# Kernel tuning notes

Hardware: AMD Instinct MI355X
Metric: run time of the kernel (lower is better)

The kernel has to match this reference:

```python
import jax, jax.numpy as jnp
import numpy as np

# ---- static config (from grid_conf / data_aug_conf) ----
B, N, C = 4, 6, 64            # batch, cameras, camC
OGH, OGW = 256, 704           # final_dim
DOWN = 16                     # 32 // up_scale
FH, FW = OGH // DOWN, OGW // DOWN   # 16, 44
DB0, DB1, DBS = 4.0, 45.0, 1.0      # dbound
D = int((DB1 - DB0) / DBS)          # 41 depth bins
DX = np.array([0.5, 0.5, 20.0], np.float32)            # dx
BX = np.array([-49.75, -49.75, 0.0], np.float32)        # bx (lower + dx/2)
NX = (200, 200, 1)                                       # nx


def make_frustum():
    # [D, FH, FW, 3] pixel (u, v, depth) frustum, matches torch create_frustum
    ds = jnp.arange(DB0, DB1, DBS, dtype=jnp.float32)[:, None, None] * jnp.ones((1, FH, FW), jnp.float32)
    xs = jnp.linspace(0.0, OGW - 1.0, FW, dtype=jnp.float32)[None, None, :] * jnp.ones((D, FH, 1), jnp.float32)
    ys = jnp.linspace(0.0, OGH - 1.0, FH, dtype=jnp.float32)[None, :, None] * jnp.ones((D, 1, FW), jnp.float32)
    return jnp.stack([xs, ys, ds], axis=-1)


def get_geometry(rots, trans, intrins, post_rots, post_trans):
    # frustum points -> ego frame, [B, N, D, FH, FW, 3]
    pts = make_frustum()[None, None] - post_trans[:, :, None, None, None, :]
    pts = jnp.einsum('bnij,bndhwj->bndhwi', jnp.linalg.inv(post_rots), pts)
    # un-project: (u*d, v*d, d)
    pts = jnp.concatenate([pts[..., :2] * pts[..., 2:3], pts[..., 2:3]], axis=-1)
    combine = rots @ jnp.linalg.inv(intrins)
    return jnp.einsum('bnij,bndhwj->bndhwi', combine, pts) + trans[:, :, None, None, None, :]


def voxel_pooling(geom, x):
    # geom: [B,N,D,H,W,3] ego coords; x: [B,N,D,H,W,C] lifted features
    dx = jnp.asarray(DX); bx = jnp.asarray(BX)
    # voxel indices; .astype(int32) truncates toward zero like torch .long()
    gi = ((geom - (bx - dx / 2.0)) / dx).astype(jnp.int32)
    Np = B * N * D * FH * FW
    gi = gi.reshape(Np, 3)
    xf = x.reshape(Np, C)
    bidx = jnp.repeat(jnp.arange(B, dtype=jnp.int32), N * D * FH * FW)
    valid = ((gi[:, 0] >= 0) & (gi[:, 0] < NX[0]) &
             (gi[:, 1] >= 0) & (gi[:, 1] < NX[1]) &
             (gi[:, 2] >= 0) & (gi[:, 2] < NX[2]))
    # flat voxel id: (((b*nz + z)*nx0 + xi)*nx1 + yi)
    flat = ((bidx * NX[2] + gi[:, 2]) * NX[0] + gi[:, 0]) * NX[1] + gi[:, 1]
    flat = jnp.where(valid, flat, 0)
    xf = xf * valid[:, None].astype(xf.dtype)
    nvox = B * NX[2] * NX[0] * NX[1]
    # scatter-add == sort + cumsum-trick per-voxel sum in the torch code
    final = jax.ops.segment_sum(xf, flat, num_segments=nvox)          # [nvox, C]
    final = final.reshape(B, NX[2], NX[0], NX[1], C)
    final = jnp.transpose(final, (0, 1, 4, 2, 3)).reshape(B, NX[2] * C, NX[0], NX[1])
    return final


def setup_inputs() -> dict:
    key = jax.random.key(0)
    k1, k2 = jax.random.split(key)
    feat_depth = jax.random.normal(k1, (B, N, D, FH, FW), jnp.float32)
    feat_pv = jax.random.normal(k2, (B, N, C, FH, FW), jnp.float32)
    # realistic 6-camera nuScenes-like rig, intrinsics scaled to 704x256
    base = np.array([[0., 0., 1.], [-1., 0., 0.], [0., -1., 0.]], np.float32)  # cam axes -> ego axes
    rots = np.zeros((B, N, 3, 3), np.float32)
    trans = np.zeros((B, N, 3), np.float32)
    for n in range(N):
        yaw = 2.0 * np.pi * n / N
        Rz = np.array([[np.cos(yaw), -np.sin(yaw), 0.], [np.sin(yaw), np.cos(yaw), 0.], [0., 0., 1.]], np.float32)
        rots[:, n] = Rz @ base
        trans[:, n] = Rz @ np.array([1.5, 0.0, 1.6], np.float32)
    fx = 1266.0 * (OGW / 1600.0)
    intr = np.array([[fx, 0., OGW / 2.0], [0., fx, OGH / 2.0], [0., 0., 1.]], np.float32)
    return {
        'feat_depth': feat_depth,
        'feat_pv': feat_pv,
        'rots': jnp.asarray(rots),
        'trans': jnp.asarray(trans),
        'intrins': jnp.asarray(np.broadcast_to(intr, (B, N, 3, 3)).copy()),
        'post_rots': jnp.asarray(np.broadcast_to(np.eye(3, dtype=np.float32), (B, N, 3, 3)).copy()),
        'post_trans': jnp.zeros((B, N, 3), jnp.float32),
    }


def reference(feat_depth, feat_pv, rots, trans, intrins, post_rots, post_trans):
    geom = get_geometry(rots, trans, intrins, post_rots, post_trans)
    geom = jax.lax.stop_gradient(geom)  # torch casts to .long(): indices are non-diff
    depth = jax.nn.softmax(feat_depth, axis=2)                 # get_depth_dist over D
    # lift: depth.unsqueeze(1) * feat.unsqueeze(2) -> [B,N,D,C,H,W] -> [B,N,D,H,W,C]
    x = depth[:, :, :, None] * feat_pv[:, :, None]
    x = jnp.transpose(x, (0, 1, 2, 4, 5, 3))
    return voxel_pooling(geom, x)                               # [B, C*nz, 200, 200]
```

## Files before the change

### kernel.cpp

```cpp
#include <hip/hip_runtime.h>
#include <math.h>

namespace {
constexpr int kB = 4, kN = 6, kC = 64, kD = 41, kFH = 16, kFW = 44;
constexpr int kNX0 = 200, kNX1 = 200;
constexpr int kHW  = kFH * kFW;
constexpr int kPix = kB * kN * kHW;
constexpr int kPts = kPix * kD;
constexpr int kVox = kB * kNX0 * kNX1;
constexpr int kPvElems = kPix * kC;
constexpr int kScanBlks = kVox / 256;
constexpr int kPvtTiles = kPix / 64;
constexpr int kSmBlks = kPix / 256;
constexpr int kFrontBlks = kPvtTiles + kSmBlks + kScanBlks;

constexpr size_t kOffPvT    = 0;
constexpr size_t kSzPvT     = (size_t)kPvElems * 4;
constexpr size_t kOffWgt    = kOffPvT + kSzPvT;
constexpr size_t kSzWgt     = (size_t)kPts * 4;
constexpr size_t kOffCnt    = kOffWgt + kSzWgt;
constexpr size_t kSzCnt     = (size_t)kVox * 4;
constexpr size_t kOffOffs   = kOffCnt + kSzCnt;
constexpr size_t kSzOffs    = 640256;
constexpr size_t kOffBSum   = kOffOffs + kSzOffs;
constexpr size_t kSzBSum    = 2560;
constexpr size_t kOffBase   = kOffBSum + kSzBSum;
constexpr size_t kSzBase    = 2560;
constexpr size_t kOffTick   = kOffBase + kSzBase;
constexpr size_t kSzTick    = 256;
constexpr size_t kOffSKW    = kOffTick + kSzTick;
constexpr size_t kSzSKW     = (size_t)kPts * 8;
constexpr size_t kWsNeed    = kOffSKW + kSzSKW + 256;
}

__device__ __forceinline__ void inv3x3(const float m[9], float inv[9]) {
    float a = m[0], b = m[1], c = m[2];
    float d = m[3], e = m[4], f = m[5];
    float g = m[6], h = m[7], i = m[8];
    float A =  (e * i - f * h);
    float Bm = -(d * i - f * g);
    float Cm =  (d * h - e * g);
    float det = a * A + b * Bm + c * Cm;
    float r = 1.0f / det;
    inv[0] = A * r;
    inv[1] = -(b * i - c * h) * r;
    inv[2] =  (b * f - c * e) * r;
    inv[3] = Bm * r;
    inv[4] =  (a * i - c * g) * r;
    inv[5] = -(a * f - c * d) * r;
    inv[6] = Cm * r;
    inv[7] = -(a * h - b * g) * r;
    inv[8] =  (a * e - b * d) * r;
}

__device__ __forceinline__ int geo_flat(int q,
                                        const float* __restrict__ rots,
                                        const float* __restrict__ trans,
                                        const float* __restrict__ intrins,
                                        const float* __restrict__ post_rots,
                                        const float* __restrict__ post_trans) {
    const int bn  = q / (kD * kHW);
    const int rem = q - bn * (kD * kHW);
    const int d   = rem / kHW;
    const int hw  = rem - d * kHW;
    const int h   = hw / kFW;
    const int w   = hw - h * kFW;
    const int b   = bn / kN;

    const float* R  = rots       + bn * 9;
    const float* K  = intrins    + bn * 9;
    const float* PR = post_rots  + bn * 9;
    const float* PT = post_trans + bn * 3;
    const float* T  = trans      + bn * 3;

    float Km[9], PRm[9];
#pragma unroll
    for (int i = 0; i < 9; ++i) { Km[i] = K[i]; PRm[i] = PR[i]; }
    float invK[9], invPR[9];
    inv3x3(Km, invK);
    inv3x3(PRm, invPR);
    float M[9];
#pragma unroll
    for (int i = 0; i < 3; ++i)
#pragma unroll
        for (int j = 0; j < 3; ++j)
            M[i * 3 + j] = R[i * 3 + 0] * invK[0 * 3 + j]
                         + R[i * 3 + 1] * invK[1 * 3 + j]
                         + R[i * 3 + 2] * invK[2 * 3 + j];

    const float u  = (float)w * (703.0f / 43.0f);
    const float v  = (float)h * 17.0f;
    const float dv = 4.0f + (float)d;
    const float px = u - PT[0], py = v - PT[1], pz = dv - PT[2];
    const float ax = invPR[0] * px + invPR[1] * py + invPR[2] * pz;
    const float ay = invPR[3] * px + invPR[4] * py + invPR[5] * pz;
    const float az = invPR[6] * px + invPR[7] * py + invPR[8] * pz;
    const float qx = ax * az, qy = ay * az, qz = az;
    const float gx = M[0] * qx + M[1] * qy + M[2] * qz + T[0];
    const float gy = M[3] * qx + M[4] * qy + M[5] * qz + T[1];
    const float gz = M[6] * qx + M[7] * qy + M[8] * qz + T[2];
    const float fx = (gx + 50.0f) / 0.5f;
    const float fy = (gy + 50.0f) / 0.5f;
    const float fz = (gz + 10.0f) / 20.0f;
    const int gix = (int)fx;
    const int giy = (int)fy;
    const int giz = (int)fz;
    if (gix >= 0 && gix < kNX0 && giy >= 0 && giy < kNX1 && giz == 0)
        return (b * kNX0 + gix) * kNX1 + giy;
    return -1;
}

__global__ __launch_bounds__(256) void lss_front(const float* __restrict__ pv,
                                                 const float* __restrict__ feat_depth,
                                                 float* __restrict__ pvT,
                                                 float* __restrict__ wgtArr,
                                                 unsigned* __restrict__ counts,
                                                 unsigned* __restrict__ ticket) {
    __shared__ float t[64][65];
    const int blk = blockIdx.x;
    const int tid = threadIdx.x;
    if (blk == 0 && tid == 0) *ticket = 0u;

    if (blk < kPvtTiles) {
        const int pix0 = blk * 64;
        const int bn  = pix0 / kHW;
        const int hw0 = pix0 - bn * kHW;
        const int lane = tid & 63;
        const int wv   = tid >> 6;
        const float* src = pv + (size_t)(bn * kC) * kHW + hw0;
#pragma unroll
        for (int cc = 0; cc < 16; ++cc) {
            const int c = wv * 16 + cc;
            t[c][lane] = src[(size_t)c * kHW + lane];
        }
        __syncthreads();
        float* dst = pvT + (size_t)pix0 * kC;
#pragma unroll
        for (int jj = 0; jj < 16; ++jj) {
            const int j = wv * 16 + jj;
            dst[j * kC + lane] = t[lane][j];
        }
    } else if (blk < kPvtTiles + kSmBlks) {
        const int pix = (blk - kPvtTiles) * 256 + tid;
        const int bn = pix / kHW;
        const int hw = pix - bn * kHW;
        const float* p = feat_depth + (size_t)(bn * kD) * kHW + hw;
        float v[kD];
#pragma unroll
        for (int d = 0; d < kD; ++d) v[d] = p[(size_t)d * kHW];
        float mx = v[0];
#pragma unroll
        for (int d = 1; d < kD; ++d) mx = fmaxf(mx, v[d]);
        float sm = 0.0f;
#pragma unroll
        for (int d = 0; d < kD; ++d) { v[d] = __expf(v[d] - mx); sm += v[d]; }
        const float inv = 1.0f / sm;
        float* o = wgtArr + (size_t)(bn * kD) * kHW + hw;
#pragma unroll
        for (int d = 0; d < kD; ++d) o[(size_t)d * kHW] = v[d] * inv;
    } else {
        const int ci = (blk - kPvtTiles - kSmBlks) * 256 + tid;
        counts[ci] = 0u;
    }
}

__global__ __launch_bounds__(256) void lss_geo(
    const float* __restrict__ rots,
    const float* __restrict__ trans,
    const float* __restrict__ intrins,
    const float* __restrict__ post_rots,
    const float* __restrict__ post_trans,
    unsigned* __restrict__ counts)
{
    const int q = blockIdx.x * 256 + threadIdx.x;
    const int f = geo_flat(q, rots, trans, intrins, post_rots, post_trans);
    if (f >= 0) atomicAdd(&counts[f], 1u);
}

__global__ __launch_bounds__(256) void lss_scan(const unsigned* __restrict__ counts,
                                                unsigned* __restrict__ offsets,
                                                unsigned* __restrict__ blockSums,
                                                unsigned* __restrict__ bases,
                                                unsigned* __restrict__ ticket) {
    __shared__ unsigned wsum[4];
    __shared__ int lastFlag;
    const int tid = threadIdx.x;
    const int i = blockIdx.x * 256 + tid;
    const int lane = tid & 63;
    const int wv = tid >> 6;

    const unsigned c = counts[i];
    unsigned s = c;
#pragma unroll
    for (int o = 1; o < 64; o <<= 1) {
        unsigned v = __shfl_up(s, o);
        if (lane >= o) s += v;
    }
    if (lane == 63) wsum[wv] = s;
    __syncthreads();
    unsigned base = 0;
#pragma unroll
    for (int k = 0; k < 3; ++k)
        if (k < wv) base += wsum[k];
    const unsigned incl = s + base;
    offsets[i] = incl - c;
    if (tid == 255) {
        atomicExch(&blockSums[blockIdx.x], incl);
        __threadfence();
    }
    __syncthreads();
    if (tid == 0)
        lastFlag = (atomicAdd(ticket, 1u) == (unsigned)(kScanBlks - 1));
    __syncthreads();
    if (!lastFlag) return;

    __threadfence();
    const int lo = tid * 3;
    const unsigned c0 = (lo     < kScanBlks) ? blockSums[lo]     : 0u;
    const unsigned c1 = (lo + 1 < kScanBlks) ? blockSums[lo + 1] : 0u;
    const unsigned c2 = (lo + 2 < kScanBlks) ? blockSums[lo + 2] : 0u;
    const unsigned t3 = c0 + c1 + c2;
    unsigned si = t3;
#pragma unroll
    for (int o = 1; o < 64; o <<= 1) {
        unsigned v = __shfl_up(si, o);
        if (lane >= o) si += v;
    }
    __syncthreads();
    if (lane == 63) wsum[wv] = si;
    __syncthreads();
    unsigned b2 = 0;
#pragma unroll
    for (int k = 0; k < 3; ++k)
        if (k < wv) b2 += wsum[k];
    unsigned run = si - t3 + b2;
    if (lo     < kScanBlks) { bases[lo]     = run; run += c0; }
    if (lo + 1 < kScanBlks) { bases[lo + 1] = run; run += c1; }
    if (lo + 2 < kScanBlks) { bases[lo + 2] = run; run += c2; }
}

__global__ __launch_bounds__(256) void lss_order(
    const float* __restrict__ rots,
    const float* __restrict__ trans,
    const float* __restrict__ intrins,
    const float* __restrict__ post_rots,
    const float* __restrict__ post_trans,
    const float* __restrict__ wgtArr,
    unsigned* __restrict__ offsets,
    const unsigned* __restrict__ bases,
    uint2* __restrict__ skw)
{
    const int q = blockIdx.x * 256 + threadIdx.x;
    const int f = geo_flat(q, rots, trans, intrins, post_rots, post_trans);
    if (f >= 0) {
        const unsigned slot = atomicAdd(&offsets[f], 1u) + bases[f >> 8];
        const int bn  = q / (kD * kHW);
        const int rem = q - bn * (kD * kHW);
        const int hw  = rem % kHW;
        uint2 u;
        u.x = (unsigned)(bn * kHW + hw);
        u.y = __float_as_uint(wgtArr[q]);
        skw[slot] = u;
    }
}

__global__ __launch_bounds__(512) void lss_gather(const float* __restrict__ pvT,
                                                  const unsigned* __restrict__ offsets,
                                                  const unsigned* __restrict__ bases,
                                                  const uint2* __restrict__ skw,
                                                  float* __restrict__ out) {
    constexpr int kChunk = 2048;
    __shared__ float acc[50][65];
    __shared__ uint2 sbuf[kChunk];
    __shared__ unsigned rowOff[51];
    const int tile = blockIdx.x;
    const int yt = tile & 3;
    const int xi = (tile >> 2) % kNX0;
    const int b  = tile / (kNX0 * 4);
    const int yi0 = yt * 50;
    const int lane = threadIdx.x & 63;
    const int wave = threadIdx.x >> 6;
    const int flat0 = (b * kNX0 + xi) * kNX1 + yi0;

    for (int e = threadIdx.x; e < 50 * 65; e += 512)
        ((float*)acc)[e] = 0.0f;
    if (threadIdx.x < 51) {
        const int f = flat0 - 1 + (int)threadIdx.x;
        rowOff[threadIdx.x] = (f < 0) ? 0u : (offsets[f] + bases[f >> 8]);
    }
    __syncthreads();

    const unsigned seg0 = rowOff[0];
    const unsigned seg1 = rowOff[50];

    for (unsigned cb = seg0; cb < seg1; cb += (unsigned)kChunk) {
        const unsigned ce = min(cb + (unsigned)kChunk, seg1);
        const int n = (int)(ce - cb);
        for (int e = threadIdx.x; e < n; e += 512)
            sbuf[e] = skw[cb + e];
        __syncthreads();

        for (int j = wave; j < 50; j += 8) {
            unsigned s0 = max(rowOff[j], cb);
            unsigned e0 = min(rowOff[j + 1], ce);
            if (s0 >= e0) continue;
            float a0 = 0.0f, a1 = 0.0f, a2 = 0.0f, a3 = 0.0f;
            int p  = (int)(s0 - cb);
            int pe = (int)(e0 - cb);
            for (; p + 8 <= pe; p += 8) {
                const uint2 u0 = sbuf[p + 0];
                const uint2 u1 = sbuf[p + 1];
                const uint2 u2 = sbuf[p + 2];
                const uint2 u3 = sbuf[p + 3];
                const uint2 u4 = sbuf[p + 4];
                const uint2 u5 = sbuf[p + 5];
                const uint2 u6 = sbuf[p + 6];
                const uint2 u7 = sbuf[p + 7];
                const float* r0 = pvT + (size_t)((unsigned)__builtin_amdgcn_readfirstlane(u0.x)) * kC;
                const float* r1 = pvT + (size_t)((unsigned)__builtin_amdgcn_readfirstlane(u1.x)) * kC;
                const float* r2 = pvT + (size_t)((unsigned)__builtin_amdgcn_readfirstlane(u2.x)) * kC;
                const float* r3 = pvT + (size_t)((unsigned)__builtin_amdgcn_readfirstlane(u3.x)) * kC;
                const float* r4 = pvT + (size_t)((unsigned)__builtin_amdgcn_readfirstlane(u4.x)) * kC;
                const float* r5 = pvT + (size_t)((unsigned)__builtin_amdgcn_readfirstlane(u5.x)) * kC;
                const float* r6 = pvT + (size_t)((unsigned)__builtin_amdgcn_readfirstlane(u6.x)) * kC;
                const float* r7 = pvT + (size_t)((unsigned)__builtin_amdgcn_readfirstlane(u7.x)) * kC;
                const float f0 = r0[lane], f1 = r1[lane], f2 = r2[lane], f3 = r3[lane];
                const float f4 = r4[lane], f5 = r5[lane], f6 = r6[lane], f7 = r7[lane];
                a0 = fmaf(__uint_as_float(__builtin_amdgcn_readfirstlane(u0.y)), f0, a0);
                a1 = fmaf(__uint_as_float(__builtin_amdgcn_readfirstlane(u1.y)), f1, a1);
                a2 = fmaf(__uint_as_float(__builtin_amdgcn_readfirstlane(u2.y)), f2, a2);
                a3 = fmaf(__uint_as_float(__builtin_amdgcn_readfirstlane(u3.y)), f3, a3);
                a0 = fmaf(__uint_as_float(__builtin_amdgcn_readfirstlane(u4.y)), f4, a0);
                a1 = fmaf(__uint_as_float(__builtin_amdgcn_readfirstlane(u5.y)), f5, a1);
                a2 = fmaf(__uint_as_float(__builtin_amdgcn_readfirstlane(u6.y)), f6, a2);
                a3 = fmaf(__uint_as_float(__builtin_amdgcn_readfirstlane(u7.y)), f7, a3);
            }
            for (; p < pe; ++p) {
                const uint2 u = sbuf[p];
                const float* r = pvT + (size_t)((unsigned)__builtin_amdgcn_readfirstlane(u.x)) * kC;
                a0 = fmaf(__uint_as_float(__builtin_amdgcn_readfirstlane(u.y)), r[lane], a0);
            }
            acc[j][lane] += (a0 + a1) + (a2 + a3);
        }
        __syncthreads();
    }
    __syncthreads();

    for (int e = threadIdx.x; e < kC * 50; e += 512) {
        const int c = e / 50, j = e % 50;
        out[((b * kC + c) * (kNX0 * kNX1)) + xi * kNX1 + yi0 + j] = acc[j][c];
    }
}

__global__ __launch_bounds__(256) void lss_scatter_fb(
    const float* __restrict__ feat_depth,
    const float* __restrict__ feat_pv,
    const float* __restrict__ rots,
    const float* __restrict__ trans,
    const float* __restrict__ intrins,
    const float* __restrict__ post_rots,
    const float* __restrict__ post_trans,
    float* __restrict__ out)
{
    const int lane = threadIdx.x & 63;
    const int wave = threadIdx.x >> 6;
    const int pix  = blockIdx.x * 4 + wave;
    const int w  = pix % kFW;
    const int h  = (pix / kFW) % kFH;
    const int bn = pix / kHW;
    const int b  = bn / kN;
    const int pixBase = h * kFW + w;
    float fd = -INFINITY;
    if (lane < kD)
        fd = feat_depth[(bn * kD + lane) * kHW + pixBase];
    float mx = fd;
#pragma unroll
    for (int off = 32; off >= 1; off >>= 1)
        mx = fmaxf(mx, __shfl_xor(mx, off));
    float ex = (lane < kD) ? __expf(fd - mx) : 0.0f;
    float sm = ex;
#pragma unroll
    for (int off = 32; off >= 1; off >>= 1)
        sm += __shfl_xor(sm, off);
    const float wgt = ex / sm;
    int vox = -1;
    if (lane < kD) {
        const int q = (bn * kD + lane) * kHW + pixBase;
        const int f = geo_flat(q, rots, trans, intrins, post_rots, post_trans);
        if (f >= 0) vox = f % (kNX0 * kNX1);
    }
    const float fc = feat_pv[(bn * kC + lane) * kHW + pixBase];
    const int outBase = (b * kC + lane) * (kNX0 * kNX1);
#pragma unroll 1
    for (int d = 0; d < kD; ++d) {
        const int   vd = __shfl(vox, d);
        const float wd = __shfl(wgt, d);
        if (vd >= 0)
            atomicAdd(&out[outBase + vd], wd * fc);
    }
}

extern "C" void kernel_launch(void* const* d_in, const int* in_sizes, int n_in,
                              void* d_out, int out_size, void* d_ws, size_t ws_size,
                              hipStream_t stream) {
    const float* feat_depth = (const float*)d_in[0];
    const float* feat_pv    = (const float*)d_in[1];
    const float* rots       = (const float*)d_in[2];
    const float* trans      = (const float*)d_in[3];
    const float* intrins    = (const float*)d_in[4];
    const float* post_rots  = (const float*)d_in[5];
    const float* post_trans = (const float*)d_in[6];
    float* out = (float*)d_out;

    if (ws_size < kWsNeed) {
        hipMemsetAsync(out, 0, (size_t)out_size * sizeof(float), stream);
        lss_scatter_fb<<<kPix / 4, 256, 0, stream>>>(
            feat_depth, feat_pv, rots, trans, intrins, post_rots, post_trans, out);
        return;
    }

    char* ws = (char*)d_ws;
    float*    pvT      = (float*)   (ws + kOffPvT);
    float*    wgtArr   = (float*)   (ws + kOffWgt);
    unsigned* counts   = (unsigned*)(ws + kOffCnt);
    unsigned* offsets  = (unsigned*)(ws + kOffOffs);
    unsigned* blockSums= (unsigned*)(ws + kOffBSum);
    unsigned* bases    = (unsigned*)(ws + kOffBase);
    unsigned* ticket   = (unsigned*)(ws + kOffTick);
    uint2*    skw      = (uint2*)   (ws + kOffSKW);

    lss_front<<<kFrontBlks, 256, 0, stream>>>(feat_pv, feat_depth, pvT, wgtArr,
                                              counts, ticket);
    lss_geo<<<kPts / 256, 256, 0, stream>>>(
        rots, trans, intrins, post_rots, post_trans, counts);
    lss_scan<<<kScanBlks, 256, 0, stream>>>(counts, offsets, blockSums, bases, ticket);
    lss_order<<<kPts / 256, 256, 0, stream>>>(
        rots, trans, intrins, post_rots, post_trans, wgtArr, offsets, bases, skw);
    lss_gather<<<kB * kNX0 * 4, 512, 0, stream>>>(pvT, offsets, bases, skw, out);
}
```

Measured before the change: 130.2 us.

## Fuse geometry counting into front kernel and cache voxel ids for ordering

The geometry/count pass is folded into the front kernel as extra blocks, and the zeroing of counts and ticket moves to a memset placed before it. The computed voxel id per point is stored in a new workspace array so the ordering kernel reads it instead of recomputing the projection. This removes one kernel launch and the duplicate geometry math. In exchange it adds a memset node and about 2.7 MB of extra global write and read traffic for the voxel-id array.

```diff
diff --git a/kernel.cpp b/kernel.cpp
--- a/kernel.cpp
+++ b/kernel.cpp
@@ -12,23 +12,26 @@
 constexpr int kScanBlks = kVox / 256;
 constexpr int kPvtTiles = kPix / 64;
 constexpr int kSmBlks = kPix / 256;
-constexpr int kFrontBlks = kPvtTiles + kSmBlks + kScanBlks;
+constexpr int kGeoBlks = kPts / 256;
+constexpr int kFrontBlks = kPvtTiles + kSmBlks + kGeoBlks;
 
 constexpr size_t kOffPvT    = 0;
 constexpr size_t kSzPvT     = (size_t)kPvElems * 4;
-constexpr size_t kOffWgt    = kOffPvT + kSzPvT;
+constexpr size_t kOffVox    = kOffPvT + kSzPvT;
+constexpr size_t kSzVox     = (size_t)kPts * 4;
+constexpr size_t kOffWgt    = kOffVox + kSzVox;
 constexpr size_t kSzWgt     = (size_t)kPts * 4;
 constexpr size_t kOffCnt    = kOffWgt + kSzWgt;
 constexpr size_t kSzCnt     = (size_t)kVox * 4;
-constexpr size_t kOffOffs   = kOffCnt + kSzCnt;
+constexpr size_t kSzTick    = 256;
+constexpr size_t kOffTick   = kOffCnt + kSzCnt;
+constexpr size_t kOffOffs   = kOffTick + kSzTick;
 constexpr size_t kSzOffs    = 640256;
 constexpr size_t kOffBSum   = kOffOffs + kSzOffs;
 constexpr size_t kSzBSum    = 2560;
 constexpr size_t kOffBase   = kOffBSum + kSzBSum;
 constexpr size_t kSzBase    = 2560;
-constexpr size_t kOffTick   = kOffBase + kSzBase;
-constexpr size_t kSzTick    = 256;
-constexpr size_t kOffSKW    = kOffTick + kSzTick;
+constexpr size_t kOffSKW    = kOffBase + kSzBase;
 constexpr size_t kSzSKW     = (size_t)kPts * 8;
 constexpr size_t kWsNeed    = kOffSKW + kSzSKW + 256;
 }
@@ -110,16 +113,22 @@
     return -1;
 }
 
-__global__ __launch_bounds__(256) void lss_front(const float* __restrict__ pv,
-                                                 const float* __restrict__ feat_depth,
-                                                 float* __restrict__ pvT,
-                                                 float* __restrict__ wgtArr,
-                                                 unsigned* __restrict__ counts,
-                                                 unsigned* __restrict__ ticket) {
+__global__ __launch_bounds__(256) void lss_front(
+    const float* __restrict__ pv,
+    const float* __restrict__ feat_depth,
+    const float* __restrict__ rots,
+    const float* __restrict__ trans,
+    const float* __restrict__ intrins,
+    const float* __restrict__ post_rots,
+    const float* __restrict__ post_trans,
+    float* __restrict__ pvT,
+    float* __restrict__ wgtArr,
+    int* __restrict__ voxArr,
+    unsigned* __restrict__ counts)
+{
     __shared__ float t[64][65];
     const int blk = blockIdx.x;
     const int tid = threadIdx.x;
-    if (blk == 0 && tid == 0) *ticket = 0u;
 
     if (blk < kPvtTiles) {
         const int pix0 = blk * 64;
@@ -159,22 +168,11 @@
 #pragma unroll
         for (int d = 0; d < kD; ++d) o[(size_t)d * kHW] = v[d] * inv;
     } else {
-        const int ci = (blk - kPvtTiles - kSmBlks) * 256 + tid;
-        counts[ci] = 0u;
-    }
-}
-
-__global__ __launch_bounds__(256) void lss_geo(
-    const float* __restrict__ rots,
-    const float* __restrict__ trans,
-    const float* __restrict__ intrins,
-    const float* __restrict__ post_rots,
-    const float* __restrict__ post_trans,
-    unsigned* __restrict__ counts)
-{
-    const int q = blockIdx.x * 256 + threadIdx.x;
-    const int f = geo_flat(q, rots, trans, intrins, post_rots, post_trans);
-    if (f >= 0) atomicAdd(&counts[f], 1u);
+        const int q = (blk - kPvtTiles - kSmBlks) * 256 + tid;
+        const int f = geo_flat(q, rots, trans, intrins, post_rots, post_trans);
+        if (f >= 0) atomicAdd(&counts[f], 1u);
+        voxArr[q] = f;
+    }
 }
 
 __global__ __launch_bounds__(256) void lss_scan(const unsigned* __restrict__ counts,
@@ -239,19 +237,13 @@
     if (lo + 2 < kScanBlks) { bases[lo + 2] = run; run += c2; }
 }
 
-__global__ __launch_bounds__(256) void lss_order(
-    const float* __restrict__ rots,
-    const float* __restrict__ trans,
-    const float* __restrict__ intrins,
-    const float* __restrict__ post_rots,
-    const float* __restrict__ post_trans,
-    const float* __restrict__ wgtArr,
-    unsigned* __restrict__ offsets,
-    const unsigned* __restrict__ bases,
-    uint2* __restrict__ skw)
-{
+__global__ __launch_bounds__(256) void lss_order(const int* __restrict__ voxArr,
+                                                 const float* __restrict__ wgtArr,
+                                                 unsigned* __restrict__ offsets,
+                                                 const unsigned* __restrict__ bases,
+                                                 uint2* __restrict__ skw) {
     const int q = blockIdx.x * 256 + threadIdx.x;
-    const int f = geo_flat(q, rots, trans, intrins, post_rots, post_trans);
+    const int f = voxArr[q];
     if (f >= 0) {
         const unsigned slot = atomicAdd(&offsets[f], 1u) + bases[f >> 8];
         const int bn  = q / (kD * kHW);
@@ -421,20 +413,21 @@
 
     char* ws = (char*)d_ws;
     float*    pvT      = (float*)   (ws + kOffPvT);
+    int*      voxArr   = (int*)     (ws + kOffVox);
     float*    wgtArr   = (float*)   (ws + kOffWgt);
     unsigned* counts   = (unsigned*)(ws + kOffCnt);
+    unsigned* ticket   = (unsigned*)(ws + kOffTick);
     unsigned* offsets  = (unsigned*)(ws + kOffOffs);
     unsigned* blockSums= (unsigned*)(ws + kOffBSum);
     unsigned* bases    = (unsigned*)(ws + kOffBase);
-    unsigned* ticket   = (unsigned*)(ws + kOffTick);
     uint2*    skw      = (uint2*)   (ws + kOffSKW);
 
-    lss_front<<<kFrontBlks, 256, 0, stream>>>(feat_pv, feat_depth, pvT, wgtArr,
-                                              counts, ticket);
-    lss_geo<<<kPts / 256, 256, 0, stream>>>(
-        rots, trans, intrins, post_rots, post_trans, counts);
+    hipMemsetAsync(counts, 0, kSzCnt + kSzTick, stream);
+
+    lss_front<<<kFrontBlks, 256, 0, stream>>>(
+        feat_pv, feat_depth, rots, trans, intrins, post_rots, post_trans,
+        pvT, wgtArr, voxArr, counts);
     lss_scan<<<kScanBlks, 256, 0, stream>>>(counts, offsets, blockSums, bases, ticket);
-    lss_order<<<kPts / 256, 256, 0, stream>>>(
-        rots, trans, intrins, post_rots, post_trans, wgtArr, offsets, bases, skw);
+    lss_order<<<kPts / 256, 256, 0, stream>>>(voxArr, wgtArr, offsets, bases, skw);
     lss_gather<<<kB * kNX0 * 4, 512, 0, stream>>>(pvT, offsets, bases, skw, out);
 }
```

Result: faster. 127.6 us (-2.0%).
